# Optimization experiments

Hardware: AMD Instinct MI355X
Metric: run time of the kernel (lower is better)

Reference implementation:

```python
import jax, jax.numpy as jnp
import numpy as np

N = 50000   # nodes
E = 800000  # edges (avg degree 16)
D = 512     # dim_h
K = 128     # truncated eigenvectors
TJ = 4      # t_number = num_J + 1
S = D // TJ # single_out (== single_out_last here)
EPS = 1e-5


def setup_inputs() -> dict:
    key = jax.random.key(0)
    ks = jax.random.split(key, 16)
    w = lambda k, sh: jax.random.normal(k, sh, jnp.float32) * 0.02
    return {
        "x": jax.random.normal(ks[0], (N, D), jnp.float32),
        "edge_index": jax.random.randint(ks[1], (2, E), 0, N, jnp.int64),
        "eigenvector": jax.random.normal(ks[2], (N, K), jnp.float32) * (N ** -0.5),
        "filter_signals": jax.random.uniform(ks[3], (1, K, TJ), jnp.float32),
        # local GCNConv(dim_h, dim_h)
        "gcn_W": w(ks[4], (D, D)), "gcn_b": jnp.zeros((D,), jnp.float32),
        # Wave_Conv_arxiv stacked lin layers [t_number, D, S]
        "lin_W": w(ks[5], (TJ, D, S)), "lin_b": jnp.zeros((TJ, S), jnp.float32),
        "fusion_W": w(ks[6], (D, D)), "fusion_b": jnp.zeros((D,), jnp.float32),
        # batch norms (training-mode batch stats)
        "bn1l_g": jnp.ones((D,), jnp.float32), "bn1l_b": jnp.zeros((D,), jnp.float32),
        "bn1a_g": jnp.ones((D,), jnp.float32), "bn1a_b": jnp.zeros((D,), jnp.float32),
        "bn2_g": jnp.ones((D,), jnp.float32), "bn2_b": jnp.zeros((D,), jnp.float32),
        # feed-forward block
        "ff1_W": w(ks[7], (D, 2 * D)), "ff1_b": jnp.zeros((2 * D,), jnp.float32),
        "ff2_W": w(ks[8], (2 * D, D)), "ff2_b": jnp.zeros((D,), jnp.float32),
    }


def _batch_norm(h, g, b):
    m = h.mean(0)
    v = ((h - m) ** 2).mean(0)
    return (h - m) * jax.lax.rsqrt(v + EPS) * g + b


def _gcn_conv(x, edge_index, W, b):
    # PyG GCNConv with symmetric normalization and added self-loops.
    src, dst = edge_index[0], edge_index[1]
    xw = x @ W  # [N, D]
    deg = jax.ops.segment_sum(jnp.ones((edge_index.shape[1],), xw.dtype), dst,
                              num_segments=x.shape[0]) + 1.0  # + self-loop
    dinv = jax.lax.rsqrt(deg)
    norm = dinv[src] * dinv[dst]  # [E]
    agg = jax.ops.segment_sum(norm[:, None] * xw[src], dst, num_segments=x.shape[0])
    agg = agg + (dinv * dinv)[:, None] * xw  # self-loop message
    return agg + b


def _wave_conv_arxiv(x, evc, filter_signals, lin_W, lin_b, fusion_W, fusion_b):
    # evc: [N, K]; filter_signals: [1, K, TJ] -> sig [TJ, K]
    sig = filter_signals[0].T[:, :, None]  # [TJ, K, 1]
    ht = jnp.einsum('nd,tds->tns', x, lin_W) + lin_b[:, None, :]  # [TJ, N, S]
    u = jnp.einsum('nk,tns->tks', evc, ht) * sig                  # [TJ, K, S]
    v = jax.nn.relu(jnp.einsum('nk,tks->tns', evc, u))            # [TJ, N, S]
    u2 = jnp.einsum('nk,tns->tks', evc, v) * sig                  # [TJ, K, S]
    out = jnp.einsum('nk,tks->tns', evc, u2)                      # [TJ, N, S]
    comb = jnp.transpose(out, (1, 0, 2)).reshape(x.shape[0], -1)  # [N, D]
    return jax.nn.relu(comb @ fusion_W + fusion_b)


def reference(x, edge_index, eigenvector, filter_signals,
              gcn_W, gcn_b, lin_W, lin_b, fusion_W, fusion_b,
              bn1l_g, bn1l_b, bn1a_g, bn1a_b, bn2_g, bn2_b,
              ff1_W, ff1_b, ff2_W, ff2_b):
    h_in = x
    # local GCN branch + residual + BN
    h_local = _gcn_conv(x, edge_index, gcn_W, gcn_b)
    h_local = _batch_norm(h_in + h_local, bn1l_g, bn1l_b)
    # global WaveGC branch + residual + BN
    h_attn = _wave_conv_arxiv(x, eigenvector, filter_signals,
                              lin_W, lin_b, fusion_W, fusion_b)
    h_attn = _batch_norm(h_in + h_attn, bn1a_g, bn1a_b)
    h = h_local + h_attn
    # feed-forward block + residual + BN
    ff = jax.nn.relu(h @ ff1_W + ff1_b) @ ff2_W + ff2_b
    h = _batch_norm(h + ff, bn2_g, bn2_b)
    return h
```

## Files before the change

kernel.cpp:

```cpp
#include <hip/hip_runtime.h>
#include <hip/hip_bf16.h>

#define NN 50000
#define DD 512
#define KE 128
#define TJN 4
#define BNEPS 1e-5f
#define ZC 64
#define KPAD 50016
#define SKE 800

typedef __attribute__((ext_vector_type(8))) short short8;
typedef __attribute__((ext_vector_type(4))) float floatx4;

__device__ __forceinline__ float bf2f(unsigned short h){
  return __uint_as_float(((unsigned int)h) << 16);
}
__device__ __forceinline__ unsigned short f2bf(float f){
  unsigned int u = __float_as_uint(f);
  unsigned int r = (u + 0x7FFF + ((u >> 16) & 1)) >> 16;
  return (unsigned short)r;
}
__device__ __forceinline__ float load1(const void* p, long i, int bf){
  if (bf) return bf2f(((const unsigned short*)p)[i]);
  return ((const float*)p)[i];
}
__device__ __forceinline__ void store1(void* p, long i, int bf, float v){
  if (bf) ((unsigned short*)p)[i] = f2bf(v);
  else ((float*)p)[i] = v;
}

typedef __attribute__((address_space(3))) unsigned int lds_uint_t;
typedef __attribute__((address_space(1))) unsigned int gbl_uint_t;
__device__ __forceinline__ void gload16(const void* gp, void* lp){
  __builtin_amdgcn_global_load_lds((const gbl_uint_t*)gp, (lds_uint_t*)lp, 16, 0, 0);
}

__global__ void detect_kernel(const void* xraw, const void* eraw, int* flags){
  if (blockIdx.x == 0 && threadIdx.x == 0){
    const unsigned short* p = (const unsigned short*)xraw;
    int cnt = 0;
    for (int i = 0; i < 128; i++){
      int e = (p[i] >> 7) & 0xFF;
      if (e >= 110 && e <= 133) cnt++;
    }
    flags[0] = (cnt >= 96) ? 1 : 0;
    const unsigned int* q = (const unsigned int*)eraw;
    int z = 0;
    for (int i = 0; i < 64; i++) if (q[2*i+1] == 0u) z++;
    flags[1] = (z >= 48) ? 1 : 0;
  }
}

struct P13 { const void* p[12]; };
__global__ void cvt_params(P13 pp, float* __restrict__ dst, const int* __restrict__ flags){
  int bf = flags[0];
  int i = blockIdx.x * 256 + threadIdx.x;
  if (i >= 6656) return;
  const void* s; int off;
  if (i < 2048){ s = pp.p[i >> 9]; off = i & 511; }
  else if (i < 3072){ s = pp.p[4]; off = i - 2048; }
  else if (i < 3584){ s = pp.p[5]; off = i - 3072; }
  else { int j = (i - 3584) >> 9; s = pp.p[6 + j]; off = (i - 3584) & 511; }
  dst[i] = load1(s, off, bf);
}

__global__ void cvt_bf(const void* __restrict__ src, unsigned short* __restrict__ dst,
                       long n, const int* __restrict__ flags){
  int bf = flags[0];
  long i = (long)blockIdx.x * blockDim.x + threadIdx.x;
  long stride = (long)gridDim.x * blockDim.x;
  if (bf){
    const unsigned short* s = (const unsigned short*)src;
    for (; i < n; i += stride) dst[i] = s[i];
  } else {
    const float* s = (const float*)src;
    for (; i < n; i += stride) dst[i] = f2bf(s[i]);
  }
}

__global__ __launch_bounds__(256) void cvt_t(
    const void* __restrict__ src, unsigned short* __restrict__ dst,
    int K, int Nc, int ldK, long srcz, long dstz, int smode,
    const int* __restrict__ flags){
  int bf = (smode == 2) ? flags[0] : smode;
  __shared__ unsigned short T[64][66];
  int bk = blockIdx.y * 64, bc = blockIdx.x * 64;
  long so = (long)blockIdx.z * srcz;
  long dof = (long)blockIdx.z * dstz;
  int tid = threadIdx.x;
#pragma unroll
  for (int p = 0; p < 16; p++){
    int idx = p * 256 + tid;
    int r = idx >> 6, c = idx & 63;
    float v = 0.f;
    if (bk + r < K) v = load1(src, so + (long)(bk + r) * Nc + bc + c, bf);
    T[r][c] = f2bf(v);
  }
  __syncthreads();
#pragma unroll
  for (int p = 0; p < 16; p++){
    int idx = p * 256 + tid;
    int r = idx >> 6, c = idx & 63;
    if (bk + c < ldK)
      dst[dof + (long)(bc + r) * ldK + bk + c] = T[c][r];
  }
}

__global__ void cvt_idx(const void* __restrict__ src, int* __restrict__ dst,
                        long n, const int* __restrict__ flags){
  int w64 = flags[1];
  long i = (long)blockIdx.x * blockDim.x + threadIdx.x;
  long stride = (long)gridDim.x * blockDim.x;
  for (; i < n; i += stride)
    dst[i] = w64 ? (int)((const long long*)src)[i] : ((const int*)src)[i];
}

__global__ void deg_kernel(const int* __restrict__ dst, int* __restrict__ deg, int E){
  int i = blockIdx.x * blockDim.x + threadIdx.x;
  if (i < E) atomicAdd(&deg[dst[i]], 1);
}

__global__ __launch_bounds__(1024) void scan_kernel(const int* __restrict__ deg,
                                                    int* __restrict__ rowptr, int E){
  __shared__ int lds[1024];
  int t = threadIdx.x;
  const int CH = (NN + 1023) / 1024;
  int base = t * CH;
  int s = 0;
  for (int i = 0; i < CH; i++){
    int idx = base + i;
    if (idx < NN) s += deg[idx];
  }
  lds[t] = s;
  __syncthreads();
  for (int off = 1; off < 1024; off <<= 1){
    int v = (t >= off) ? lds[t - off] : 0;
    __syncthreads();
    lds[t] += v;
    __syncthreads();
  }
  int ex = (t == 0) ? 0 : lds[t - 1];
  for (int i = 0; i < CH; i++){
    int idx = base + i;
    if (idx < NN){ rowptr[idx] = ex; ex += deg[idx]; }
  }
  if (t == 1023) rowptr[NN] = ex;
}

__global__ void dinv_kernel(const int* __restrict__ deg, float* __restrict__ dinv){
  int i = blockIdx.x * blockDim.x + threadIdx.x;
  if (i < NN) dinv[i] = rsqrtf((float)deg[i] + 1.0f);
}

__global__ void scatter_kernel(const int* __restrict__ srcv, const int* __restrict__ dstv,
                               const int* __restrict__ rowptr, int* __restrict__ cursor,
                               int* __restrict__ csr, int E){
  int i = blockIdx.x * blockDim.x + threadIdx.x;
  if (i < E){
    int d = dstv[i];
    int pos = atomicAdd(&cursor[d], 1);
    csr[rowptr[d] + pos] = srcv[i];
  }
}

__global__ __launch_bounds__(64) void gcn_gather(
    const int* __restrict__ rowptr, const int* __restrict__ csr,
    const float* __restrict__ dinv, const void* __restrict__ xw ,
    const void* __restrict__ X, const float* __restrict__ bias,
    float* __restrict__ out, const int* __restrict__ flags){
  int d = blockIdx.x;
  int lane = threadIdx.x;
  __shared__ int s_idx[64];
  __shared__ float s_dv[64];
  int start = rowptr[d], end = rowptr[d + 1];
  float dd = dinv[d];
  float acc[8];
#pragma unroll
  for (int k = 0; k < 8; k++) acc[k] = 0.f;
  const unsigned short* xwp = (const unsigned short*)xw;
  int c0 = lane * 8;
  for (int j0 = start; j0 < end; j0 += 64){
    int cnt = min(64, end - j0);
    __syncthreads();
    if (lane < cnt){
      int s = csr[j0 + lane];
      s_idx[lane] = s;
      s_dv[lane] = dinv[s];
    }
    __syncthreads();
    for (int t = 0; t < cnt; t++){
      int s = s_idx[t];
      float nm = dd * s_dv[t];
      union { float4 f; unsigned short u[8]; } r;
      r.f = *(const float4*)(xwp + (long)s * DD + c0);
#pragma unroll
      for (int k = 0; k < 8; k++) acc[k] += nm * bf2f(r.u[k]);
    }
  }
  int xf = flags[0];
  long base = (long)d * DD + c0;
  union { float4 f; unsigned short u[8]; } sf;
  sf.f = *(const float4*)(xwp + base);
  float d2 = dd * dd;
#pragma unroll
  for (int k = 0; k < 8; k++)
    out[base + k] = load1(X, base + k, xf) + acc[k] + d2 * bf2f(sf.u[k]) + bias[c0 + k];
}

__global__ __launch_bounds__(512) void bn_stats(const float* __restrict__ T,
                                                float* __restrict__ sum,
                                                float* __restrict__ sumsq){
  int c = threadIdx.x;
  long r0 = (long)blockIdx.x * 128;
  float s = 0.f, q = 0.f;
  for (int r = 0; r < 128; r++){
    long rr = r0 + r;
    if (rr < NN){
      float v = T[rr * DD + c];
      s += v; q += v * v;
    }
  }
  atomicAdd(&sum[c], s);
  atomicAdd(&sumsq[c], q);
}

__global__ void bn_apply(const float* __restrict__ T,
                         const float* __restrict__ sum, const float* __restrict__ sumsq,
                         const float* __restrict__ g, const float* __restrict__ b,
                         const void* __restrict__ addsrc, int addmode,
                         void* __restrict__ out, int outmode,
                         unsigned short* __restrict__ out2,
                         const int* __restrict__ flags){
  int am = (addmode == 2) ? flags[0] : addmode;
  int om = (outmode == 2) ? flags[0] : outmode;
  long i = (long)blockIdx.x * blockDim.x + threadIdx.x;
  long stride = (long)gridDim.x * blockDim.x;
  long n = (long)NN * DD;
  const float invN = 1.0f / (float)NN;
  for (; i < n; i += stride){
    int c = (int)(i & 511);
    float m = sum[c] * invN;
    float var = sumsq[c] * invN - m * m;
    float v = (T[i] - m) * rsqrtf(var + BNEPS) * g[c] + b[c];
    if (addsrc) v += load1(addsrc, i, am);
    store1(out, i, om, v);
    if (out2) out2[i] = f2bf(v);
  }
}

__global__ void scale_sig_t(const float* __restrict__ U, const float* __restrict__ filt,
                            unsigned short* __restrict__ Ut){
  int i = blockIdx.x * blockDim.x + threadIdx.x;
  if (i < KE * DD){
    int k = i >> 9;
    int c = i & 511;
    float v = U[i] * filt[k * TJN + (c >> 7)];
    Ut[(long)c * KE + k] = f2bf(v);
  }
}

__global__ void zero_out_bf16(void* out, long nbytes){
  long i = (long)blockIdx.x * blockDim.x + threadIdx.x;
  long stride = (long)gridDim.x * blockDim.x;
  long n = nbytes / 2;
  for (; i < n; i += stride) ((unsigned short*)out)[i] = 0;
}

__global__ __launch_bounds__(256) void gemm_mfma(
    const unsigned short* __restrict__ A, const unsigned short* __restrict__ Bt,
    void* __restrict__ C, int M, int N, int Kd, int lda, int ldc,
    const float* __restrict__ bias, const void* __restrict__ addsrc, int dorelu,
    int addmode, int cmode, const int* __restrict__ flags){
  int fl = flags[0];
  int adbf = (addmode == 2) ? fl : addmode;
  int cbf = (cmode == 2) ? fl : cmode;
  __shared__ unsigned short Asl[128 * 32];
  __shared__ unsigned short Bsl[128 * 32];
  const int tid = threadIdx.x;

  int nx = gridDim.x;
  int nwg = nx * gridDim.y;
  int p = blockIdx.y * nx + blockIdx.x;
  int q8 = nwg >> 3, r8 = nwg & 7;
  int xcd = p & 7, off = p >> 3;
  int id = (xcd < r8 ? xcd * (q8 + 1) : r8 * (q8 + 1) + (xcd - r8) * q8) + off;
  int by = id / nx, bx = id - by * nx;
  const int bm = by * 128, bn = bx * 128;

  const int lane = tid & 63, wave = tid >> 6;
  const int wm = (wave & 1) * 64, wn = (wave >> 1) * 64;
  const int q = lane >> 4, l16 = lane & 15;
  const int swz = (q ^ ((l16 >> 1) & 3)) << 3;
  floatx4 acc[4][4];
#pragma unroll
  for (int i = 0; i < 4; i++)
#pragma unroll
    for (int j = 0; j < 4; j++)
#pragma unroll
      for (int r = 0; r < 4; r++) acc[i][j][r] = 0.f;

  const int sbase = wave << 7;

  for (int k0 = 0; k0 < Kd; k0 += 32){
    __syncthreads();
#pragma unroll
    for (int pp = 0; pp < 2; pp++){
      int slot = sbase + (pp << 6) + lane;
      int row = slot >> 2;
      int ssl = (slot & 3) ^ ((slot >> 3) & 3);
      int rA = bm + row; if (rA > M - 1) rA = M - 1;
      unsigned short* ldst_a = &Asl[(sbase + (pp << 6)) << 3];
      unsigned short* ldst_b = &Bsl[(sbase + (pp << 6)) << 3];
      gload16(A + (long)rA * lda + k0 + (ssl << 3), ldst_a);
      gload16(Bt + (long)(bn + row) * Kd + k0 + (ssl << 3), ldst_b);
    }
    __syncthreads();
    short8 af[4], bfr[4];
#pragma unroll
    for (int i = 0; i < 4; i++){
      int ra = wm + i * 16 + l16;
      af[i] = *(const short8*)&Asl[(ra << 5) + swz];
      int rb = wn + i * 16 + l16;
      bfr[i] = *(const short8*)&Bsl[(rb << 5) + swz];
    }
#pragma unroll
    for (int i = 0; i < 4; i++)
#pragma unroll
      for (int j = 0; j < 4; j++)
        acc[i][j] = __builtin_amdgcn_mfma_f32_16x16x32_bf16(af[i], bfr[j], acc[i][j], 0, 0, 0);
  }
#pragma unroll
  for (int i = 0; i < 4; i++){
#pragma unroll
    for (int r = 0; r < 4; r++){
      int row = bm + wm + i * 16 + q * 4 + r;
      if (row >= M) continue;
#pragma unroll
      for (int j = 0; j < 4; j++){
        int col = bn + wn + j * 16 + l16;
        float v = acc[i][j][r];
        if (bias) v += bias[col];
        if (dorelu) v = fmaxf(v, 0.f);
        if (addsrc) v += load1(addsrc, (long)row * ldc + col, adbf);
        store1(C, (long)row * ldc + col, cbf, v);
      }
    }
  }
}

__global__ __launch_bounds__(256) void gemm_mfma_t(
    const unsigned short* __restrict__ A, const unsigned short* __restrict__ Bt,
    unsigned short* __restrict__ Ct, int M, int Kd, int lda, int ldct,
    const float* __restrict__ bias, int dorelu){
  __shared__ unsigned short Asl[128 * 32];
  __shared__ unsigned short Bsl[128 * 32];
  __shared__ unsigned short sc[128 * 132];
  const int tid = threadIdx.x;

  int nx = gridDim.x;
  int nwg = nx * gridDim.y;
  int p = blockIdx.y * nx + blockIdx.x;
  int q8 = nwg >> 3, r8 = nwg & 7;
  int xcd = p & 7, off = p >> 3;
  int id = (xcd < r8 ? xcd * (q8 + 1) : r8 * (q8 + 1) + (xcd - r8) * q8) + off;
  int by = id / nx, bx = id - by * nx;
  const int bm = by * 128, bn = bx * 128;

  const int lane = tid & 63, wave = tid >> 6;
  const int wm = (wave & 1) * 64, wn = (wave >> 1) * 64;
  const int q = lane >> 4, l16 = lane & 15;
  const int swz = (q ^ ((l16 >> 1) & 3)) << 3;
  floatx4 acc[4][4];
#pragma unroll
  for (int i = 0; i < 4; i++)
#pragma unroll
    for (int j = 0; j < 4; j++)
#pragma unroll
      for (int r = 0; r < 4; r++) acc[i][j][r] = 0.f;

  const int sbase = wave << 7;

  for (int k0 = 0; k0 < Kd; k0 += 32){
    __syncthreads();
#pragma unroll
    for (int pp = 0; pp < 2; pp++){
      int slot = sbase + (pp << 6) + lane;
      int row = slot >> 2;
      int ssl = (slot & 3) ^ ((slot >> 3) & 3);
      int rA = bm + row; if (rA > M - 1) rA = M - 1;
      unsigned short* ldst_a = &Asl[(sbase + (pp << 6)) << 3];
      unsigned short* ldst_b = &Bsl[(sbase + (pp << 6)) << 3];
      gload16(A + (long)rA * lda + k0 + (ssl << 3), ldst_a);
      gload16(Bt + (long)(bn + row) * Kd + k0 + (ssl << 3), ldst_b);
    }
    __syncthreads();
    short8 af[4], bfr[4];
#pragma unroll
    for (int i = 0; i < 4; i++){
      int ra = wm + i * 16 + l16;
      af[i] = *(const short8*)&Asl[(ra << 5) + swz];
      int rb = wn + i * 16 + l16;
      bfr[i] = *(const short8*)&Bsl[(rb << 5) + swz];
    }
#pragma unroll
    for (int i = 0; i < 4; i++)
#pragma unroll
      for (int j = 0; j < 4; j++)
        acc[i][j] = __builtin_amdgcn_mfma_f32_16x16x32_bf16(af[i], bfr[j], acc[i][j], 0, 0, 0);
  }
#pragma unroll
  for (int i = 0; i < 4; i++){
#pragma unroll
    for (int j = 0; j < 4; j++){
      int lr0 = wm + i * 16 + q * 4;
      int lc = wn + j * 16 + l16;
      float v0 = acc[i][j][0], v1 = acc[i][j][1], v2 = acc[i][j][2], v3 = acc[i][j][3];
      if (bias){ float bb = bias[bn + lc]; v0 += bb; v1 += bb; v2 += bb; v3 += bb; }
      if (dorelu){
        v0 = fmaxf(v0, 0.f); v1 = fmaxf(v1, 0.f);
        v2 = fmaxf(v2, 0.f); v3 = fmaxf(v3, 0.f);
      }
      ushort4 pk;
      pk.x = f2bf(v0); pk.y = f2bf(v1); pk.z = f2bf(v2); pk.w = f2bf(v3);
      *(ushort4*)&sc[lc * 132 + lr0] = pk;
    }
  }
  __syncthreads();
#pragma unroll
  for (int pp = 0; pp < 8; pp++){
    int idx = pp * 2048 + tid * 8;
    int r2 = idx >> 7, c2 = idx & 127;
    int gc = bm + c2;
    if (gc >= ldct) continue;
    short8 o;
#pragma unroll
    for (int e = 0; e < 8; e++)
      ((unsigned short*)&o)[e] = (gc + e < M) ? sc[r2 * 132 + c2 + e] : (unsigned short)0;
    *(short8*)&Ct[(long)(bn + r2) * ldct + gc] = o;
  }
}

__global__ __launch_bounds__(256) void gemm_sk(
    const unsigned short* __restrict__ A, const unsigned short* __restrict__ Bt,
    float* __restrict__ P, int ldk){
  __shared__ unsigned short Asl[128 * 32];
  __shared__ unsigned short Bsl[128 * 32];
  const int tid = threadIdx.x;
  const int bn = blockIdx.x * 128;
  const int ks = blockIdx.z * SKE;
  const int ke = min(ks + SKE, KPAD);

  const int lane = tid & 63, wave = tid >> 6;
  const int wm = (wave & 1) * 64, wn = (wave >> 1) * 64;
  const int q = lane >> 4, l16 = lane & 15;
  const int swz = (q ^ ((l16 >> 1) & 3)) << 3;
  floatx4 acc[4][4];
#pragma unroll
  for (int i = 0; i < 4; i++)
#pragma unroll
    for (int j = 0; j < 4; j++)
#pragma unroll
      for (int r = 0; r < 4; r++) acc[i][j][r] = 0.f;

  const int sbase = wave << 7;

  for (int k0 = ks; k0 < ke; k0 += 32){
    __syncthreads();
#pragma unroll
    for (int pp = 0; pp < 2; pp++){
      int slot = sbase + (pp << 6) + lane;
      int row = slot >> 2;
      int ssl = (slot & 3) ^ ((slot >> 3) & 3);
      unsigned short* ldst_a = &Asl[(sbase + (pp << 6)) << 3];
      unsigned short* ldst_b = &Bsl[(sbase + (pp << 6)) << 3];
      gload16(A + (long)row * ldk + k0 + (ssl << 3), ldst_a);
      gload16(Bt + (long)(bn + row) * ldk + k0 + (ssl << 3), ldst_b);
    }
    __syncthreads();
    short8 af[4], bfr[4];
#pragma unroll
    for (int i = 0; i < 4; i++){
      int ra = wm + i * 16 + l16;
      af[i] = *(const short8*)&Asl[(ra << 5) + swz];
      int rb = wn + i * 16 + l16;
      bfr[i] = *(const short8*)&Bsl[(rb << 5) + swz];
    }
#pragma unroll
    for (int i = 0; i < 4; i++)
#pragma unroll
      for (int j = 0; j < 4; j++)
        acc[i][j] = __builtin_amdgcn_mfma_f32_16x16x32_bf16(af[i], bfr[j], acc[i][j], 0, 0, 0);
  }
  long base = (long)blockIdx.z * (KE * DD);
#pragma unroll
  for (int i = 0; i < 4; i++){
#pragma unroll
    for (int r = 0; r < 4; r++){
      int row = wm + i * 16 + q * 4 + r;
#pragma unroll
      for (int j = 0; j < 4; j++){
        int col = bn + wn + j * 16 + l16;
        P[base + (long)row * DD + col] = acc[i][j][r];
      }
    }
  }
}

__global__ void reduce_part(const float* __restrict__ P, float* __restrict__ C){
  int i = blockIdx.x * 256 + threadIdx.x;
  float s = 0.f;
  for (int z = 0; z < ZC; z++) s += P[(long)z * (KE * DD) + i];
  C[i] = s;
}

__global__ __launch_bounds__(256) void evsum_kernel(const unsigned short* __restrict__ EVb,
                                                    float* __restrict__ evsum){
  int b = blockIdx.x, t = threadIdx.x;
  int k = t & 127, half = t >> 7;
  float s = 0.f;
  for (int r = 0; r < 128; r += 2){
    int row = b * 128 + r + half;
    if (row < NN) s += bf2f(EVb[(long)row * KE + k]);
  }
  atomicAdd(&evsum[k], s);
}

__global__ __launch_bounds__(256) void wave_mix(
    const float* __restrict__ XU, const unsigned short* __restrict__ W2t,
    const float* __restrict__ evsum, const float* __restrict__ b2,
    const float* __restrict__ filt, unsigned short* __restrict__ Ut){
  int i = blockIdx.x * 256 + threadIdx.x;
  int k = i >> 9, c = i & 511;
  float acc = evsum[k] * b2[c];
  const float* xr = XU + (long)k * DD;
  const unsigned short* wr = W2t + (long)c * DD;
#pragma unroll 4
  for (int d = 0; d < DD; d += 8){
    float4 x0 = *(const float4*)(xr + d);
    float4 x1 = *(const float4*)(xr + d + 4);
    ushort4 w0 = *(const ushort4*)(wr + d);
    ushort4 w1 = *(const ushort4*)(wr + d + 4);
    acc += x0.x * bf2f(w0.x) + x0.y * bf2f(w0.y) + x0.z * bf2f(w0.z) + x0.w * bf2f(w0.w)
         + x1.x * bf2f(w1.x) + x1.y * bf2f(w1.y) + x1.z * bf2f(w1.z) + x1.w * bf2f(w1.w);
  }
  float v = acc * filt[k * TJN + (c >> 7)];
  Ut[(long)c * KE + k] = f2bf(v);
}

extern "C" void kernel_launch(void* const* d_in, const int* in_sizes, int n_in,
                              void* d_out, int out_size, void* d_ws, size_t ws_size,
                              hipStream_t stream){
  const int E = in_sizes[1] / 2;
  const long NB = (long)NN * DD;
  float* ws = (float*)d_ws;
  (void)n_in;

  size_t cur = 0;
  auto alloc = [&](size_t n){ size_t o = cur; cur += (n + 63) & ~(size_t)63; return o; };

  size_t o_flags = alloc(64);
  size_t o_zero  = cur;
  size_t o_U     = alloc((size_t)KE * DD);
  size_t o_U2    = alloc((size_t)KE * DD);
  size_t o_stats = alloc(6 * DD);
  size_t o_evsum = alloc(KE);
  size_t o_ideg  = alloc(NN);
  size_t o_cur   = alloc(NN);
  size_t zlen    = cur - o_zero;
  size_t o_dinv  = alloc(NN);
  size_t o_rowp  = alloc(NN + 64);
  size_t o_filt  = alloc(KE * TJN);
  size_t o_bgcn  = alloc(DD);
  size_t o_b2    = alloc(DD);
  size_t o_bfus  = alloc(DD);
  size_t o_bff1  = alloc(2 * DD);
  size_t o_bff2  = alloc(DD);
  size_t o_bn    = alloc(6 * DD);
  size_t o_Wgt   = alloc((size_t)DD * DD / 2);
  size_t o_W2t   = alloc((size_t)DD * DD / 2);
  size_t o_Wft   = alloc((size_t)DD * DD / 2);
  size_t o_W1t   = alloc((size_t)DD * DD);
  size_t o_Wff2t = alloc((size_t)DD * DD);
  size_t o_Ut    = alloc((size_t)KE * DD / 2);
  size_t o_U2t   = alloc((size_t)KE * DD / 2);
  size_t o_idx   = alloc((size_t)2 * E);
  size_t o_csr   = alloc((size_t)E);
  size_t o_part  = alloc((size_t)ZC * KE * DD);
  size_t o_BF    = alloc(NB);
  size_t o_BA    = alloc(NB / 2);
  size_t o_BHL   = alloc(NB / 2);
  size_t o_Xb    = alloc(NB / 2);
  size_t o_EVb   = alloc((size_t)NN * KE / 2);
  size_t o_Hb    = alloc(NB / 2);

  if (cur * 4 > ws_size){
    zero_out_bf16<<<2048, 256, 0, stream>>>(d_out, (long)out_size * 2);
    return;
  }

  int* flags = (int*)(ws + o_flags);
  float* BF  = ws + o_BF;
  void* BA   = (void*)(ws + o_BA);
  void* BHL  = (void*)(ws + o_BHL);
  void* F1   = BA;
  int* srcv  = (int*)(ws + o_idx);
  int* dstv  = srcv + E;
  int* ideg  = (int*)(ws + o_ideg);
  int* cursor= (int*)(ws + o_cur);
  int* rowp  = (int*)(ws + o_rowp);
  int* csr   = (int*)(ws + o_csr);
  float* dinv= ws + o_dinv;
  float* U   = ws + o_U;
  float* U2  = ws + o_U2;
  float* st  = ws + o_stats;
  float* Part= ws + o_part;
  unsigned short* Wgt   = (unsigned short*)(ws + o_Wgt);
  unsigned short* W2t   = (unsigned short*)(ws + o_W2t);
  unsigned short* Wft   = (unsigned short*)(ws + o_Wft);
  unsigned short* W1t   = (unsigned short*)(ws + o_W1t);
  unsigned short* Wff2t = (unsigned short*)(ws + o_Wff2t);
  unsigned short* Ut    = (unsigned short*)(ws + o_Ut);
  unsigned short* U2t   = (unsigned short*)(ws + o_U2t);
  unsigned short* Xb    = (unsigned short*)(ws + o_Xb);
  unsigned short* EVb   = (unsigned short*)(ws + o_EVb);
  unsigned short* Hb    = (unsigned short*)(ws + o_Hb);
  unsigned short* XbT  = (unsigned short*)(ws + o_BF);
  unsigned short* EVbT = (unsigned short*)(ws + o_BF + 12804160);
  unsigned short* VAt  = (unsigned short*)BA;

  detect_kernel<<<1, 64, 0, stream>>>(d_in[0], d_in[1], flags);
  hipMemsetAsync(ws + o_zero, 0, zlen * 4, stream);

  P13 pp;
  pp.p[0] = d_in[3];  pp.p[1] = d_in[5];  pp.p[2] = d_in[7];  pp.p[3] = d_in[9];
  pp.p[4] = d_in[17]; pp.p[5] = d_in[19];
  for (int i = 0; i < 6; i++) pp.p[6 + i] = d_in[10 + i];
  cvt_params<<<26, 256, 0, stream>>>(pp, ws + o_filt, flags);

  cvt_bf<<<4096, 256, 0, stream>>>(d_in[0], Xb, NB, flags);
  cvt_bf<<<2048, 256, 0, stream>>>(d_in[2], EVb, (long)NN * KE, flags);
  cvt_t<<<dim3(8, 8),   256, 0, stream>>>(d_in[4],  Wgt,   DD, DD, DD, 0, 0, 2, flags);
  cvt_t<<<dim3(2, 8, 4),256, 0, stream>>>(d_in[6],  W2t,   DD, 128, DD,
                                          (long)DD * 128, (long)128 * DD, 2, flags);
  cvt_t<<<dim3(8, 8),   256, 0, stream>>>(d_in[8],  Wft,   DD, DD, DD, 0, 0, 2, flags);
  cvt_t<<<dim3(16, 8),  256, 0, stream>>>(d_in[16], W1t,   DD, 2 * DD, DD, 0, 0, 2, flags);
  cvt_t<<<dim3(8, 16),  256, 0, stream>>>(d_in[18], Wff2t, 2 * DD, DD, 2 * DD, 0, 0, 2, flags);
  cvt_t<<<dim3(8, 782), 256, 0, stream>>>(Xb,  XbT,  NN, DD, KPAD, 0, 0, 1, flags);
  cvt_t<<<dim3(2, 782), 256, 0, stream>>>(EVb, EVbT, NN, KE, KPAD, 0, 0, 1, flags);
  cvt_idx<<<4096, 256, 0, stream>>>(d_in[1], srcv, 2L * E, flags);

  deg_kernel<<<(E + 255) / 256, 256, 0, stream>>>(dstv, ideg, E);
  scan_kernel<<<1, 1024, 0, stream>>>(ideg, rowp, E);
  dinv_kernel<<<(NN + 255) / 256, 256, 0, stream>>>(ideg, dinv);
  scatter_kernel<<<(E + 255) / 256, 256, 0, stream>>>(srcv, dstv, rowp, cursor, csr, E);

  const int MT = (NN + 127) / 128;
  dim3 blk(256);
  const void* Xr = d_in[0];

  gemm_sk<<<dim3(4, 1, ZC), blk, 0, stream>>>(EVbT, XbT, Part, KPAD);
  reduce_part<<<256, 256, 0, stream>>>(Part, U);
  evsum_kernel<<<MT, 256, 0, stream>>>(EVb, ws + o_evsum);
  wave_mix<<<256, 256, 0, stream>>>(U, W2t, ws + o_evsum, ws + o_b2,
                                    ws + o_filt, Ut);
  gemm_mfma_t<<<dim3(4, MT), blk, 0, stream>>>(EVb, Ut, VAt, NN, KE, KE, KPAD,
                                               nullptr, 1);
  gemm_sk<<<dim3(4, 1, ZC), blk, 0, stream>>>(EVbT, VAt, Part, KPAD);
  reduce_part<<<256, 256, 0, stream>>>(Part, U2);
  scale_sig_t<<<(KE * DD) / 256, 256, 0, stream>>>(U2, ws + o_filt, U2t);
  gemm_mfma<<<dim3(4, MT), blk, 0, stream>>>(EVb, U2t, BA, NN, DD, KE, KE, DD,
                                             nullptr, nullptr, 0, 0, 1, flags);
  gemm_mfma<<<dim3(4, MT), blk, 0, stream>>>((const unsigned short*)BA, Wft, BF,
                                             NN, DD, DD, DD, DD,
                                             ws + o_bfus, Xr, 1, 2, 0, flags);
  bn_stats<<<MT, 512, 0, stream>>>(BF, st + 2 * DD, st + 3 * DD);
  bn_apply<<<4096, 256, 0, stream>>>(BF, st + 2 * DD, st + 3 * DD,
                                     ws + o_bn + 2 * DD, ws + o_bn + 3 * DD,
                                     nullptr, 0, BHL, 1, nullptr, flags);

  gemm_mfma<<<dim3(4, MT), blk, 0, stream>>>(Xb, Wgt, BA, NN, DD, DD, DD, DD,
                                             nullptr, nullptr, 0, 0, 1, flags);
  gcn_gather<<<NN, 64, 0, stream>>>(rowp, csr, dinv, BA, Xr, ws + o_bgcn, BF, flags);
  bn_stats<<<MT, 512, 0, stream>>>(BF, st + 0, st + DD);
  bn_apply<<<4096, 256, 0, stream>>>(BF, st + 0, st + DD,
                                     ws + o_bn + 0 * DD, ws + o_bn + 1 * DD,
                                     BHL, 1, BF, 0, Hb, flags);

  gemm_mfma<<<dim3(8, MT), blk, 0, stream>>>(Hb, W1t, F1, NN, 2 * DD, DD, DD, 2 * DD,
                                             ws + o_bff1, nullptr, 1, 0, 1, flags);
  gemm_mfma<<<dim3(4, MT), blk, 0, stream>>>((const unsigned short*)F1, Wff2t, BF,
                                             NN, DD, 2 * DD, 2 * DD, DD,
                                             ws + o_bff2, BF, 0, 0, 0, flags);
  bn_stats<<<MT, 512, 0, stream>>>(BF, st + 4 * DD, st + 5 * DD);
  bn_apply<<<4096, 256, 0, stream>>>(BF, st + 4 * DD, st + 5 * DD,
                                     ws + o_bn + 4 * DD, ws + o_bn + 5 * DD,
                                     nullptr, 0, d_out, 2, nullptr, flags);
}
```

Baseline: 1.766 ms.

## Fold fusion weight into eigen-projection, fuse bf16 conversion with transpose, deepen GEMM K-tile

Reassociates the final wave projection so that (evc·(sig∘U2))·Wf becomes evc·((sig∘U2)·Wf). A small mix2 kernel precomputes the K×D product, which removes one full N×D×D GEMM and the intermediate N×D buffer. The bf16 conversion and the transposes of X and the eigenvectors are merged into a single pass, cutting redundant global traffic. The MFMA GEMMs now stage 64-wide K tiles with a new XOR swizzle and share LDS with the epilogue, which halves the barrier count but uses more LDS per block and may lower occupancy.

```diff
diff --git a/kernel.cpp b/kernel.cpp
--- a/kernel.cpp
+++ b/kernel.cpp
@@ -65,17 +65,32 @@
   dst[i] = load1(s, off, bf);
 }
 
-__global__ void cvt_bf(const void* __restrict__ src, unsigned short* __restrict__ dst,
-                       long n, const int* __restrict__ flags){
+__global__ __launch_bounds__(256) void cvt_bt(
+    const void* __restrict__ src, unsigned short* __restrict__ dst1,
+    unsigned short* __restrict__ dst2, int K, int Nc, int ldK,
+    const int* __restrict__ flags){
   int bf = flags[0];
-  long i = (long)blockIdx.x * blockDim.x + threadIdx.x;
-  long stride = (long)gridDim.x * blockDim.x;
-  if (bf){
-    const unsigned short* s = (const unsigned short*)src;
-    for (; i < n; i += stride) dst[i] = s[i];
-  } else {
-    const float* s = (const float*)src;
-    for (; i < n; i += stride) dst[i] = f2bf(s[i]);
+  __shared__ unsigned short T[64][66];
+  int bk = blockIdx.y * 64, bc = blockIdx.x * 64;
+  int tid = threadIdx.x;
+#pragma unroll
+  for (int p = 0; p < 16; p++){
+    int idx = p * 256 + tid;
+    int r = idx >> 6, c = idx & 63;
+    unsigned short h = 0;
+    if (bk + r < K){
+      h = f2bf(load1(src, (long)(bk + r) * Nc + bc + c, bf));
+      dst1[(long)(bk + r) * Nc + bc + c] = h;
+    }
+    T[r][c] = h;
+  }
+  __syncthreads();
+#pragma unroll
+  for (int p = 0; p < 16; p++){
+    int idx = p * 256 + tid;
+    int r = idx >> 6, c = idx & 63;
+    if (bk + c < ldK)
+      dst2[(long)(bc + r) * ldK + bk + c] = T[c][r];
   }
 }
 
@@ -249,17 +264,6 @@
   }
 }
 
-__global__ void scale_sig_t(const float* __restrict__ U, const float* __restrict__ filt,
-                            unsigned short* __restrict__ Ut){
-  int i = blockIdx.x * blockDim.x + threadIdx.x;
-  if (i < KE * DD){
-    int k = i >> 9;
-    int c = i & 511;
-    float v = U[i] * filt[k * TJN + (c >> 7)];
-    Ut[(long)c * KE + k] = f2bf(v);
-  }
-}
-
 __global__ void zero_out_bf16(void* out, long nbytes){
   long i = (long)blockIdx.x * blockDim.x + threadIdx.x;
   long stride = (long)gridDim.x * blockDim.x;
@@ -275,8 +279,8 @@
   int fl = flags[0];
   int adbf = (addmode == 2) ? fl : addmode;
   int cbf = (cmode == 2) ? fl : cmode;
-  __shared__ unsigned short Asl[128 * 32];
-  __shared__ unsigned short Bsl[128 * 32];
+  __shared__ unsigned short Asl[128 * 64];
+  __shared__ unsigned short Bsl[128 * 64];
   const int tid = threadIdx.x;
 
   int nx = gridDim.x;
@@ -291,7 +295,6 @@
   const int lane = tid & 63, wave = tid >> 6;
   const int wm = (wave & 1) * 64, wn = (wave >> 1) * 64;
   const int q = lane >> 4, l16 = lane & 15;
-  const int swz = (q ^ ((l16 >> 1) & 3)) << 3;
   floatx4 acc[4][4];
 #pragma unroll
   for (int i = 0; i < 4; i++)
@@ -300,35 +303,36 @@
 #pragma unroll
       for (int r = 0; r < 4; r++) acc[i][j][r] = 0.f;
 
-  const int sbase = wave << 7;
-
-  for (int k0 = 0; k0 < Kd; k0 += 32){
-    __syncthreads();
-#pragma unroll
-    for (int pp = 0; pp < 2; pp++){
+  const int sbase = wave << 8;
+
+  for (int k0 = 0; k0 < Kd; k0 += 64){
+    __syncthreads();
+#pragma unroll
+    for (int pp = 0; pp < 4; pp++){
       int slot = sbase + (pp << 6) + lane;
-      int row = slot >> 2;
-      int ssl = (slot & 3) ^ ((slot >> 3) & 3);
+      int row = slot >> 3;
+      int ssl = (slot & 7) ^ (row & 7);
       int rA = bm + row; if (rA > M - 1) rA = M - 1;
-      unsigned short* ldst_a = &Asl[(sbase + (pp << 6)) << 3];
-      unsigned short* ldst_b = &Bsl[(sbase + (pp << 6)) << 3];
-      gload16(A + (long)rA * lda + k0 + (ssl << 3), ldst_a);
-      gload16(Bt + (long)(bn + row) * Kd + k0 + (ssl << 3), ldst_b);
-    }
-    __syncthreads();
-    short8 af[4], bfr[4];
-#pragma unroll
-    for (int i = 0; i < 4; i++){
-      int ra = wm + i * 16 + l16;
-      af[i] = *(const short8*)&Asl[(ra << 5) + swz];
-      int rb = wn + i * 16 + l16;
-      bfr[i] = *(const short8*)&Bsl[(rb << 5) + swz];
-    }
-#pragma unroll
-    for (int i = 0; i < 4; i++)
-#pragma unroll
-      for (int j = 0; j < 4; j++)
-        acc[i][j] = __builtin_amdgcn_mfma_f32_16x16x32_bf16(af[i], bfr[j], acc[i][j], 0, 0, 0);
+      gload16(A + (long)rA * lda + k0 + (ssl << 3), &Asl[(sbase + (pp << 6)) << 3]);
+      gload16(Bt + (long)(bn + row) * Kd + k0 + (ssl << 3), &Bsl[(sbase + (pp << 6)) << 3]);
+    }
+    __syncthreads();
+#pragma unroll
+    for (int kk = 0; kk < 2; kk++){
+      short8 af[4], bfr[4];
+#pragma unroll
+      for (int i = 0; i < 4; i++){
+        int ra = wm + i * 16 + l16;
+        af[i] = *(const short8*)&Asl[(ra << 6) + ((((kk << 2) + q) ^ (ra & 7)) << 3)];
+        int rb = wn + i * 16 + l16;
+        bfr[i] = *(const short8*)&Bsl[(rb << 6) + ((((kk << 2) + q) ^ (rb & 7)) << 3)];
+      }
+#pragma unroll
+      for (int i = 0; i < 4; i++)
+#pragma unroll
+        for (int j = 0; j < 4; j++)
+          acc[i][j] = __builtin_amdgcn_mfma_f32_16x16x32_bf16(af[i], bfr[j], acc[i][j], 0, 0, 0);
+    }
   }
 #pragma unroll
   for (int i = 0; i < 4; i++){
@@ -353,9 +357,9 @@
     const unsigned short* __restrict__ A, const unsigned short* __restrict__ Bt,
     unsigned short* __restrict__ Ct, int M, int Kd, int lda, int ldct,
     const float* __restrict__ bias, int dorelu){
-  __shared__ unsigned short Asl[128 * 32];
-  __shared__ unsigned short Bsl[128 * 32];
-  __shared__ unsigned short sc[128 * 132];
+  __shared__ unsigned short lds[16896];
+  unsigned short* Asl = lds;
+  unsigned short* Bsl = lds + 8192;
   const int tid = threadIdx.x;
 
   int nx = gridDim.x;
@@ -370,7 +374,6 @@
   const int lane = tid & 63, wave = tid >> 6;
   const int wm = (wave & 1) * 64, wn = (wave >> 1) * 64;
   const int q = lane >> 4, l16 = lane & 15;
-  const int swz = (q ^ ((l16 >> 1) & 3)) << 3;
   floatx4 acc[4][4];
 #pragma unroll
   for (int i = 0; i < 4; i++)
@@ -379,36 +382,38 @@
 #pragma unroll
       for (int r = 0; r < 4; r++) acc[i][j][r] = 0.f;
 
-  const int sbase = wave << 7;
-
-  for (int k0 = 0; k0 < Kd; k0 += 32){
-    __syncthreads();
-#pragma unroll
-    for (int pp = 0; pp < 2; pp++){
+  const int sbase = wave << 8;
+
+  for (int k0 = 0; k0 < Kd; k0 += 64){
+    __syncthreads();
+#pragma unroll
+    for (int pp = 0; pp < 4; pp++){
       int slot = sbase + (pp << 6) + lane;
-      int row = slot >> 2;
-      int ssl = (slot & 3) ^ ((slot >> 3) & 3);
+      int row = slot >> 3;
+      int ssl = (slot & 7) ^ (row & 7);
       int rA = bm + row; if (rA > M - 1) rA = M - 1;
-      unsigned short* ldst_a = &Asl[(sbase + (pp << 6)) << 3];
-      unsigned short* ldst_b = &Bsl[(sbase + (pp << 6)) << 3];
-      gload16(A + (long)rA * lda + k0 + (ssl << 3), ldst_a);
-      gload16(Bt + (long)(bn + row) * Kd + k0 + (ssl << 3), ldst_b);
-    }
-    __syncthreads();
-    short8 af[4], bfr[4];
-#pragma unroll
-    for (int i = 0; i < 4; i++){
-      int ra = wm + i * 16 + l16;
-      af[i] = *(const short8*)&Asl[(ra << 5) + swz];
-      int rb = wn + i * 16 + l16;
-      bfr[i] = *(const short8*)&Bsl[(rb << 5) + swz];
-    }
-#pragma unroll
-    for (int i = 0; i < 4; i++)
-#pragma unroll
-      for (int j = 0; j < 4; j++)
-        acc[i][j] = __builtin_amdgcn_mfma_f32_16x16x32_bf16(af[i], bfr[j], acc[i][j], 0, 0, 0);
-  }
+      gload16(A + (long)rA * lda + k0 + (ssl << 3), &Asl[(sbase + (pp << 6)) << 3]);
+      gload16(Bt + (long)(bn + row) * Kd + k0 + (ssl << 3), &Bsl[(sbase + (pp << 6)) << 3]);
+    }
+    __syncthreads();
+#pragma unroll
+    for (int kk = 0; kk < 2; kk++){
+      short8 af[4], bfr[4];
+#pragma unroll
+      for (int i = 0; i < 4; i++){
+        int ra = wm + i * 16 + l16;
+        af[i] = *(const short8*)&Asl[(ra << 6) + ((((kk << 2) + q) ^ (ra & 7)) << 3)];
+        int rb = wn + i * 16 + l16;
+        bfr[i] = *(const short8*)&Bsl[(rb << 6) + ((((kk << 2) + q) ^ (rb & 7)) << 3)];
+      }
+#pragma unroll
+      for (int i = 0; i < 4; i++)
+#pragma unroll
+        for (int j = 0; j < 4; j++)
+          acc[i][j] = __builtin_amdgcn_mfma_f32_16x16x32_bf16(af[i], bfr[j], acc[i][j], 0, 0, 0);
+    }
+  }
+  __syncthreads();
 #pragma unroll
   for (int i = 0; i < 4; i++){
 #pragma unroll
@@ -423,7 +428,7 @@
       }
       ushort4 pk;
       pk.x = f2bf(v0); pk.y = f2bf(v1); pk.z = f2bf(v2); pk.w = f2bf(v3);
-      *(ushort4*)&sc[lc * 132 + lr0] = pk;
+      *(ushort4*)&lds[lc * 132 + lr0] = pk;
     }
   }
   __syncthreads();
@@ -436,7 +441,7 @@
     short8 o;
 #pragma unroll
     for (int e = 0; e < 8; e++)
-      ((unsigned short*)&o)[e] = (gc + e < M) ? sc[r2 * 132 + c2 + e] : (unsigned short)0;
+      ((unsigned short*)&o)[e] = (gc + e < M) ? lds[r2 * 132 + c2 + e] : (unsigned short)0;
     *(short8*)&Ct[(long)(bn + r2) * ldct + gc] = o;
   }
 }
@@ -472,10 +477,8 @@
       int slot = sbase + (pp << 6) + lane;
       int row = slot >> 2;
       int ssl = (slot & 3) ^ ((slot >> 3) & 3);
-      unsigned short* ldst_a = &Asl[(sbase + (pp << 6)) << 3];
-      unsigned short* ldst_b = &Bsl[(sbase + (pp << 6)) << 3];
-      gload16(A + (long)row * ldk + k0 + (ssl << 3), ldst_a);
-      gload16(Bt + (long)(bn + row) * ldk + k0 + (ssl << 3), ldst_b);
+      gload16(A + (long)row * ldk + k0 + (ssl << 3), &Asl[(sbase + (pp << 6)) << 3]);
+      gload16(Bt + (long)(bn + row) * ldk + k0 + (ssl << 3), &Bsl[(sbase + (pp << 6)) << 3]);
     }
     __syncthreads();
     short8 af[4], bfr[4];
@@ -546,6 +549,32 @@
   }
   float v = acc * filt[k * TJN + (c >> 7)];
   Ut[(long)c * KE + k] = f2bf(v);
+}
+
+__global__ __launch_bounds__(256) void mix2(
+    const float* __restrict__ U2, const unsigned short* __restrict__ Wft,
+    const float* __restrict__ filt, unsigned short* __restrict__ M2t){
+  int i = blockIdx.x * 256 + threadIdx.x;
+  int k = i & 127, j = i >> 7;
+  float fs0 = filt[k * TJN + 0], fs1 = filt[k * TJN + 1];
+  float fs2 = filt[k * TJN + 2], fs3 = filt[k * TJN + 3];
+  const float* ur = U2 + (long)k * DD;
+  const unsigned short* wr = Wft + (long)j * DD;
+  float acc = 0.f;
+#pragma unroll
+  for (int t = 0; t < 4; t++){
+    float a = 0.f;
+    for (int c = t * 128; c < t * 128 + 128; c += 8){
+      float4 x0 = *(const float4*)(ur + c);
+      float4 x1 = *(const float4*)(ur + c + 4);
+      ushort4 w0 = *(const ushort4*)(wr + c);
+      ushort4 w1 = *(const ushort4*)(wr + c + 4);
+      a += x0.x * bf2f(w0.x) + x0.y * bf2f(w0.y) + x0.z * bf2f(w0.z) + x0.w * bf2f(w0.w)
+         + x1.x * bf2f(w1.x) + x1.y * bf2f(w1.y) + x1.z * bf2f(w1.z) + x1.w * bf2f(w1.w);
+    }
+    acc += (t == 0 ? fs0 : t == 1 ? fs1 : t == 2 ? fs2 : fs3) * a;
+  }
+  M2t[(long)j * KE + k] = f2bf(acc);
 }
 
 extern "C" void kernel_launch(void* const* d_in, const int* in_sizes, int n_in,
@@ -583,7 +612,7 @@
   size_t o_W1t   = alloc((size_t)DD * DD);
   size_t o_Wff2t = alloc((size_t)DD * DD);
   size_t o_Ut    = alloc((size_t)KE * DD / 2);
-  size_t o_U2t   = alloc((size_t)KE * DD / 2);
+  size_t o_M2t   = alloc((size_t)KE * DD / 2);
   size_t o_idx   = alloc((size_t)2 * E);
   size_t o_csr   = alloc((size_t)E);
   size_t o_part  = alloc((size_t)ZC * KE * DD);
@@ -621,7 +650,7 @@
   unsigned short* W1t   = (unsigned short*)(ws + o_W1t);
   unsigned short* Wff2t = (unsigned short*)(ws + o_Wff2t);
   unsigned short* Ut    = (unsigned short*)(ws + o_Ut);
-  unsigned short* U2t   = (unsigned short*)(ws + o_U2t);
+  unsigned short* M2t   = (unsigned short*)(ws + o_M2t);
   unsigned short* Xb    = (unsigned short*)(ws + o_Xb);
   unsigned short* EVb   = (unsigned short*)(ws + o_EVb);
   unsigned short* Hb    = (unsigned short*)(ws + o_Hb);
@@ -638,16 +667,14 @@
   for (int i = 0; i < 6; i++) pp.p[6 + i] = d_in[10 + i];
   cvt_params<<<26, 256, 0, stream>>>(pp, ws + o_filt, flags);
 
-  cvt_bf<<<4096, 256, 0, stream>>>(d_in[0], Xb, NB, flags);
-  cvt_bf<<<2048, 256, 0, stream>>>(d_in[2], EVb, (long)NN * KE, flags);
+  cvt_bt<<<dim3(8, 782), 256, 0, stream>>>(d_in[0], Xb,  XbT,  NN, DD, KPAD, flags);
+  cvt_bt<<<dim3(2, 782), 256, 0, stream>>>(d_in[2], EVb, EVbT, NN, KE, KPAD, flags);
   cvt_t<<<dim3(8, 8),   256, 0, stream>>>(d_in[4],  Wgt,   DD, DD, DD, 0, 0, 2, flags);
   cvt_t<<<dim3(2, 8, 4),256, 0, stream>>>(d_in[6],  W2t,   DD, 128, DD,
                                           (long)DD * 128, (long)128 * DD, 2, flags);
   cvt_t<<<dim3(8, 8),   256, 0, stream>>>(d_in[8],  Wft,   DD, DD, DD, 0, 0, 2, flags);
   cvt_t<<<dim3(16, 8),  256, 0, stream>>>(d_in[16], W1t,   DD, 2 * DD, DD, 0, 0, 2, flags);
   cvt_t<<<dim3(8, 16),  256, 0, stream>>>(d_in[18], Wff2t, 2 * DD, DD, 2 * DD, 0, 0, 2, flags);
-  cvt_t<<<dim3(8, 782), 256, 0, stream>>>(Xb,  XbT,  NN, DD, KPAD, 0, 0, 1, flags);
-  cvt_t<<<dim3(2, 782), 256, 0, stream>>>(EVb, EVbT, NN, KE, KPAD, 0, 0, 1, flags);
   cvt_idx<<<4096, 256, 0, stream>>>(d_in[1], srcv, 2L * E, flags);
 
   deg_kernel<<<(E + 255) / 256, 256, 0, stream>>>(dstv, ideg, E);
@@ -668,11 +695,8 @@
                                                nullptr, 1);
   gemm_sk<<<dim3(4, 1, ZC), blk, 0, stream>>>(EVbT, VAt, Part, KPAD);
   reduce_part<<<256, 256, 0, stream>>>(Part, U2);
-  scale_sig_t<<<(KE * DD) / 256, 256, 0, stream>>>(U2, ws + o_filt, U2t);
-  gemm_mfma<<<dim3(4, MT), blk, 0, stream>>>(EVb, U2t, BA, NN, DD, KE, KE, DD,
-                                             nullptr, nullptr, 0, 0, 1, flags);
-  gemm_mfma<<<dim3(4, MT), blk, 0, stream>>>((const unsigned short*)BA, Wft, BF,
-                                             NN, DD, DD, DD, DD,
+  mix2<<<256, 256, 0, stream>>>(U2, Wft, ws + o_filt, M2t);
+  gemm_mfma<<<dim3(4, MT), blk, 0, stream>>>(EVb, M2t, BF, NN, DD, KE, KE, DD,
                                              ws + o_bfus, Xr, 1, 2, 0, flags);
   bn_stats<<<MT, 512, 0, stream>>>(BF, st + 2 * DD, st + 3 * DD);
   bn_apply<<<4096, 256, 0, stream>>>(BF, st + 2 * DD, st + 3 * DD,
```

New measurement: 1.828 ms. 3.5% more time.
